# Performance work log

Hardware: AMD Instinct MI355X
Metric: run time of the kernel (lower is better)

Reference implementation:

```python
import jax, jax.numpy as jnp
import numpy as np

MEAN = jnp.array([0.4914, 0.4822, 0.4465], dtype=jnp.float32)
STD = jnp.array([0.2023, 0.1994, 0.201], dtype=jnp.float32)


def conv2d(x, w, b, stride, pad):
    out = jax.lax.conv_general_dilated(
        x, w, (stride, stride), [(pad, pad), (pad, pad)],
        dimension_numbers=('NCHW', 'OIHW', 'NCHW'))
    return out + b[None, :, None, None]


def topk_select(out_list, scores):
    # SubNet zeros the lowest int(0.75*N) |scores|; SelectNet gathers the
    # surviving channels in original channel order.
    N = scores.shape[1]
    keep = N - int(0.75 * N)
    _, idx = jax.lax.top_k(scores, keep)
    idx = jnp.sort(idx, axis=1)  # boolean-mask gather preserves order
    if out_list.ndim == 4:
        return jnp.take_along_axis(out_list, idx[:, :, None, None], axis=1)
    return jnp.take_along_axis(out_list, idx, axis=1)


def moe_conv(x, We, be, Wr, br, stride, pad):
    B = x.shape[0]
    out = conv2d(x, We.reshape((-1,) + We.shape[2:]), be.reshape(-1), stride, pad)
    scores = jnp.abs(x.reshape(B, -1) @ Wr + br)
    return topk_select(out, scores)


def moe_linear(x, We, be, Wr, br):
    out = (jnp.einsum('bi,eoi->beo', x, We) + be[None]).reshape(x.shape[0], -1)
    scores = jnp.abs(x @ Wr + br)
    return topk_select(out, scores)


def setup_inputs():
    key = jax.random.key(0)
    ks = iter(jax.random.split(key, 32))

    def w(shape, fan_in):
        return jax.random.normal(next(ks), shape, jnp.float32) / np.sqrt(fan_in)

    B = 1024
    inp = {'x': jax.random.uniform(next(ks), (B, 3, 32, 32), jnp.float32)}
    inp['W0'] = w((32, 3, 3, 3), 27);        inp['b0'] = jnp.zeros((32,), jnp.float32)
    inp['W2'] = w((32, 32, 4, 4), 512);      inp['b2'] = jnp.zeros((32,), jnp.float32)
    inp['W4'] = w((64, 32, 3, 3), 288);      inp['b4'] = jnp.zeros((64,), jnp.float32)
    inp['W6e'] = w((4, 64, 64, 4, 4), 1024); inp['b6e'] = jnp.zeros((4, 64), jnp.float32)
    inp['Wr6'] = w((64 * 16 * 16, 256), 16384); inp['br6'] = jnp.zeros((256,), jnp.float32)
    inp['W9e'] = w((4, 512, 4096), 4096);    inp['b9e'] = jnp.zeros((4, 512), jnp.float32)
    inp['Wr9'] = w((4096, 2048), 4096);      inp['br9'] = jnp.zeros((2048,), jnp.float32)
    inp['W11e'] = w((4, 512, 512), 512);     inp['b11e'] = jnp.zeros((4, 512), jnp.float32)
    inp['Wr11'] = w((512, 2048), 512);       inp['br11'] = jnp.zeros((2048,), jnp.float32)
    inp['W13e'] = w((4, 10, 512), 512);      inp['b13e'] = jnp.zeros((4, 10), jnp.float32)
    inp['Wr13'] = w((512, 40), 512);         inp['br13'] = jnp.zeros((40,), jnp.float32)
    return inp


def reference(x, W0, b0, W2, b2, W4, b4,
              W6e, b6e, Wr6, br6,
              W9e, b9e, Wr9, br9,
              W11e, b11e, Wr11, br11,
              W13e, b13e, Wr13, br13):
    x = (x - MEAN[None, :, None, None]) / STD[None, :, None, None]
    out = jax.nn.relu(conv2d(x, W0, b0, 1, 1))      # [B,32,32,32]
    out = jax.nn.relu(conv2d(out, W2, b2, 2, 1))    # [B,32,16,16]
    out = jax.nn.relu(conv2d(out, W4, b4, 1, 1))    # [B,64,16,16]
    out = jax.nn.relu(moe_conv(out, W6e, b6e, Wr6, br6, 2, 1))  # [B,64,8,8]
    out = out.reshape(out.shape[0], -1)             # [B,4096]
    out = jax.nn.relu(moe_linear(out, W9e, b9e, Wr9, br9))      # [B,512]
    out = jax.nn.relu(moe_linear(out, W11e, b11e, Wr11, br11))  # [B,512]
    return moe_linear(out, W13e, b13e, Wr13, br13)  # [B,10]
```

## Files before the change

kernel.cpp:

```cpp
#include <hip/hip_runtime.h>
#include <stdint.h>

#define DEV __device__ __forceinline__

typedef __attribute__((ext_vector_type(8))) short bf16x8;
typedef __attribute__((ext_vector_type(8))) unsigned short u16x8;
typedef __attribute__((ext_vector_type(4))) float f32x4;

DEV unsigned short rne1(float f, float& rem) {
  uint32_t u = __float_as_uint(f);
  uint32_t t = (u + 0x7fffu + ((u >> 16) & 1u)) & 0xffff0000u;
  rem = f - __uint_as_float(t);
  return (unsigned short)(t >> 16);
}
DEV void split3(float f, unsigned short& a0, unsigned short& a1, unsigned short& a2) {
  float r1, r2;
  a0 = rne1(f, r1);
  a1 = rne1(r1, r2);
  uint32_t u = __float_as_uint(r2);
  a2 = (unsigned short)((u + 0x7fffu + ((u >> 16) & 1u)) >> 16);
}
DEV void split3_4(float4 v, ushort4& h0, ushort4& h1, ushort4& h2) {
  split3(v.x, h0.x, h1.x, h2.x);
  split3(v.y, h0.y, h1.y, h2.y);
  split3(v.z, h0.z, h1.z, h2.z);
  split3(v.w, h0.w, h1.w, h2.w);
}

__global__ __launch_bounds__(256) void k_conv0(
    const float* __restrict__ x, const float* __restrict__ W,
    const float* __restrict__ b, float* __restrict__ y0, int base)
{
  __shared__ float sIn[3][34][34];
  const int t = threadIdx.x;
  const long img = base + blockIdx.x;
  const float mean[3] = {0.4914f, 0.4822f, 0.4465f};
  const float stdv[3] = {0.2023f, 0.1994f, 0.201f};
  for (int i = t; i < 3 * 34 * 34; i += 256) {
    int c = i / 1156, r = i % 1156, yy = r / 34 - 1, xx = r % 34 - 1;
    float v = 0.f;
    if ((unsigned)yy < 32u && (unsigned)xx < 32u)
      v = (x[((img * 3 + c) * 32 + yy) * 32 + xx] - mean[c]) / stdv[c];
    (&sIn[0][0][0])[i] = v;
  }
  __syncthreads();
  for (int p = t; p < 1024; p += 256) {
    const int py = p >> 5, px = p & 31;
    float in[27];
#pragma unroll
    for (int c = 0; c < 3; c++)
#pragma unroll
      for (int ky = 0; ky < 3; ky++)
#pragma unroll
        for (int kx = 0; kx < 3; kx++)
          in[c * 9 + ky * 3 + kx] = sIn[c][py + ky][px + kx];
#pragma unroll 4
    for (int oc = 0; oc < 32; oc++) {
      float acc = b[oc];
      const float* wp = W + oc * 27;
#pragma unroll
      for (int k = 0; k < 27; k++) acc += in[k] * wp[k];
      y0[(((long)blockIdx.x * 32 + oc) * 32 + py) * 32 + px] = fmaxf(acc, 0.f);
    }
  }
}

__global__ __launch_bounds__(256, 4) void k_conv2(
    const float* __restrict__ y0, const float* __restrict__ W,
    const float* __restrict__ b, float* __restrict__ y2)
{
  __shared__ float sP[2][2][8][17][17];
  const int t = threadIdx.x;
  const int px = t & 15, py = t >> 4;
  float acc[32];
#pragma unroll
  for (int o = 0; o < 32; o++) acc[o] = b[o];
  for (int icp = 0; icp < 4; icp++) {
    __syncthreads();
    for (int i = t; i < 8 * 34 * 34; i += 256) {
      int c = i / 1156, r = i % 1156, iy = r / 34 - 1, ix = r % 34 - 1;
      float v = 0.f;
      if ((unsigned)iy < 32u && (unsigned)ix < 32u)
        v = y0[(((long)blockIdx.x * 32 + icp * 8 + c) * 32 + iy) * 32 + ix];
      sP[iy & 1][ix & 1][c][(iy + 1) >> 1][(ix + 1) >> 1] = v;
    }
    __syncthreads();
#pragma unroll 1
    for (int c = 0; c < 8; c++) {
      float in[16];
#pragma unroll
      for (int ky = 0; ky < 4; ky++)
#pragma unroll
        for (int kx = 0; kx < 4; kx++)
          in[ky * 4 + kx] = sP[(ky + 1) & 1][(kx + 1) & 1][c][py + (ky >> 1)][px + (kx >> 1)];
      const float* wp = W + (icp * 8 + c) * 16;
#pragma unroll
      for (int o = 0; o < 32; o++) {
        float s = 0.f;
#pragma unroll
        for (int k = 0; k < 16; k++)
          s += in[k] * wp[o * 512 + k];
        acc[o] += s;
      }
    }
  }
#pragma unroll
  for (int o = 0; o < 32; o++)
    y2[(((long)blockIdx.x * 32 + o) * 16 + py) * 16 + px] = fmaxf(acc[o], 0.f);
}

__global__ __launch_bounds__(256) void k_splitW4(
    const float* __restrict__ W, unsigned short* __restrict__ Wsp)
{
  const int i = blockIdx.x * 256 + threadIdx.x;
  if (i >= 64 * 288) return;
  const int o = i / 288, r = i % 288, ic = r / 9, tap = r % 9;
  unsigned short a0, a1, a2;
  split3(W[i], a0, a1, a2);
  const int base = (tap * 64 + o) * 32 + ic;
  Wsp[base] = a0;
  Wsp[18432 + base] = a1;
  Wsp[36864 + base] = a2;
}

__global__ __launch_bounds__(256, 2) void k_conv4m(
    const float* __restrict__ y2, const unsigned short* __restrict__ Wsp,
    const float* __restrict__ bb, float* __restrict__ y4)
{
  __shared__ __align__(16) unsigned short sX[3][324][40];
  const int t = threadIdx.x;
  const int lane = t & 63, wid = t >> 6;
  const int fr = lane & 15, kg = lane >> 4;
  const long img = blockIdx.x;
  const float* yimg = y2 + img * (32 * 256);

  for (int i = t; i < 324 * 32; i += 256) {
    const int ic = i / 324, pos = i % 324;
    const int iy = pos / 18, ix = pos % 18;
    float v = 0.f;
    if ((unsigned)(iy - 1) < 16u && (unsigned)(ix - 1) < 16u)
      v = yimg[(ic * 16 + iy - 1) * 16 + ix - 1];
    unsigned short a0, a1, a2;
    split3(v, a0, a1, a2);
    sX[0][pos][ic] = a0;
    sX[1][pos][ic] = a1;
    sX[2][pos][ic] = a2;
  }
  __syncthreads();

  f32x4 acc[4][4];
#pragma unroll
  for (int i = 0; i < 4; i++)
#pragma unroll
    for (int j = 0; j < 4; j++) acc[i][j] = (f32x4)0.f;

  const int pyb = wid * 4;
#pragma unroll 1
  for (int tap = 0; tap < 9; tap++) {
    const int ky = tap / 3, kx = tap % 3;
    bf16x8 bfv[3][4];
#pragma unroll
    for (int s = 0; s < 3; s++)
#pragma unroll
      for (int nf = 0; nf < 4; nf++)
        bfv[s][nf] = *(const bf16x8*)&sX[s][(pyb + nf + ky) * 18 + fr + kx][kg * 8];
#pragma unroll
    for (int mf = 0; mf < 4; mf++) {
      const int wb = (tap * 64 + mf * 16 + fr) * 32 + kg * 8;
      bf16x8 a0 = *(const bf16x8*)&Wsp[wb];
      bf16x8 a1 = *(const bf16x8*)&Wsp[18432 + wb];
      bf16x8 a2 = *(const bf16x8*)&Wsp[36864 + wb];
#pragma unroll
      for (int nf = 0; nf < 4; nf++) {
        f32x4 a = acc[mf][nf];
        a = __builtin_amdgcn_mfma_f32_16x16x32_bf16(a1, bfv[1][nf], a, 0, 0, 0);
        a = __builtin_amdgcn_mfma_f32_16x16x32_bf16(a0, bfv[2][nf], a, 0, 0, 0);
        a = __builtin_amdgcn_mfma_f32_16x16x32_bf16(a2, bfv[0][nf], a, 0, 0, 0);
        a = __builtin_amdgcn_mfma_f32_16x16x32_bf16(a1, bfv[0][nf], a, 0, 0, 0);
        a = __builtin_amdgcn_mfma_f32_16x16x32_bf16(a0, bfv[1][nf], a, 0, 0, 0);
        a = __builtin_amdgcn_mfma_f32_16x16x32_bf16(a0, bfv[0][nf], a, 0, 0, 0);
        acc[mf][nf] = a;
      }
    }
  }
#pragma unroll
  for (int mf = 0; mf < 4; mf++)
#pragma unroll
    for (int nf = 0; nf < 4; nf++) {
      const int p2 = wid * 64 + nf * 16 + fr;
#pragma unroll
      for (int reg = 0; reg < 4; reg++) {
        const int oc = mf * 16 + kg * 4 + reg;
        y4[(img * 64 + oc) * 256 + p2] = fmaxf(acc[mf][nf][reg] + bb[oc], 0.f);
      }
    }
}

__global__ __launch_bounds__(256) void k_splitW(
    const float* __restrict__ W, unsigned short* __restrict__ Wsp)
{
  const int i = (blockIdx.x * 256 + threadIdx.x) * 4;
  float4 v = *(const float4*)&W[i];
  ushort4 h0, h1, h2; split3_4(v, h0, h1, h2);
  *(ushort4*)&Wsp[i]          = h0;
  *(ushort4*)&Wsp[262144 + i] = h1;
  *(ushort4*)&Wsp[524288 + i] = h2;
}

__global__ __launch_bounds__(256) void k_conv6m(
    const float* __restrict__ y4, const unsigned short* __restrict__ Wsp,
    const float* __restrict__ bb, float* __restrict__ c6)
{
  __shared__ __align__(16) unsigned short sB[3][64][56];
  const int t = threadIdx.x;
  const int lane = t & 63, wid = t >> 6;
  const int fr = lane & 15, kg = lane >> 4;
  const long img = blockIdx.x;
  const int pix = t >> 2, q = t & 3;
  const int spy = pix >> 3, spx = pix & 7;
  const int icL = q >> 1, kyB = (q & 1) * 2;
  const float* yimg = y4 + img * (64 * 256);

  f32x4 acc[4][4];
#pragma unroll
  for (int i = 0; i < 4; i++)
#pragma unroll
    for (int j = 0; j < 4; j++) acc[i][j] = (f32x4)0.f;

#pragma unroll 1
  for (int ks = 0; ks < 32; ks++) {
    const int ic = ks * 2 + icL;
    float v[8];
#pragma unroll
    for (int j = 0; j < 8; j++) {
      const int ky = kyB + (j >> 2), kx = j & 3;
      const int iy = 2 * spy + ky - 1, ix = 2 * spx + kx - 1;
      v[j] = ((unsigned)iy < 16u && (unsigned)ix < 16u)
               ? yimg[(ic * 16 + iy) * 16 + ix] : 0.f;
    }
    u16x8 h0, h1, h2;
#pragma unroll
    for (int j = 0; j < 8; j++) {
      unsigned short a0, a1, a2;
      split3(v[j], a0, a1, a2);
      h0[j] = a0; h1[j] = a1; h2[j] = a2;
    }
    __syncthreads();
    *(u16x8*)&sB[0][pix][q * 8] = h0;
    *(u16x8*)&sB[1][pix][q * 8] = h1;
    *(u16x8*)&sB[2][pix][q * 8] = h2;
    __syncthreads();

    bf16x8 bfv[3][4];
#pragma unroll
    for (int s = 0; s < 3; s++)
#pragma unroll
      for (int nf = 0; nf < 4; nf++)
        bfv[s][nf] = *(const bf16x8*)&sB[s][nf * 16 + fr][kg * 8];

    const int kbase = ks * 32 + kg * 8;
#pragma unroll
    for (int mf = 0; mf < 4; mf++) {
      const int oc = wid * 64 + mf * 16 + fr;
      bf16x8 a0 = *(const bf16x8*)&Wsp[(long)oc * 1024 + kbase];
      bf16x8 a1 = *(const bf16x8*)&Wsp[(long)(256 + oc) * 1024 + kbase];
      bf16x8 a2 = *(const bf16x8*)&Wsp[(long)(512 + oc) * 1024 + kbase];
#pragma unroll
      for (int nf = 0; nf < 4; nf++) {
        f32x4 a = acc[mf][nf];
        a = __builtin_amdgcn_mfma_f32_16x16x32_bf16(a1, bfv[1][nf], a, 0, 0, 0);
        a = __builtin_amdgcn_mfma_f32_16x16x32_bf16(a0, bfv[2][nf], a, 0, 0, 0);
        a = __builtin_amdgcn_mfma_f32_16x16x32_bf16(a2, bfv[0][nf], a, 0, 0, 0);
        a = __builtin_amdgcn_mfma_f32_16x16x32_bf16(a1, bfv[0][nf], a, 0, 0, 0);
        a = __builtin_amdgcn_mfma_f32_16x16x32_bf16(a0, bfv[1][nf], a, 0, 0, 0);
        a = __builtin_amdgcn_mfma_f32_16x16x32_bf16(a0, bfv[0][nf], a, 0, 0, 0);
        acc[mf][nf] = a;
      }
    }
  }
#pragma unroll
  for (int mf = 0; mf < 4; mf++)
#pragma unroll
    for (int nf = 0; nf < 4; nf++) {
      const int ocb = wid * 64 + mf * 16 + kg * 4;
      const int p2 = nf * 16 + fr;
#pragma unroll
      for (int reg = 0; reg < 4; reg++) {
        const int oc = ocb + reg;
        c6[(img * 256 + oc) * 64 + p2] = acc[mf][nf][reg] + bb[oc];
      }
    }
}

template<int B_NK, int DO_ABS, int SPLITK>
__global__ __launch_bounds__(256, 4) void k_sgemm(
    const float* __restrict__ A, const float* __restrict__ Bm,
    const float* __restrict__ bias, float* __restrict__ C,
    int M, int N, int K)
{
  __shared__ float As[16][68];
  __shared__ float Bs[16][68];
  const int t = threadIdx.x;
  const int tx = t & 15, ty = t >> 4;
  const int n0 = blockIdx.x * 64, m0 = blockIdx.y * 64;
  const int Kc = K / SPLITK;
  const int k0 = blockIdx.z * Kc;
  float acc[4][4] = {{0.f}};
  for (int kt = 0; kt < Kc; kt += 16) {
    __syncthreads();
    {
      const int kc = t & 15, r0 = t >> 4;
#pragma unroll
      for (int i = 0; i < 4; i++)
        As[kc][r0 + 16 * i] = A[(long)(m0 + r0 + 16 * i) * K + k0 + kt + kc];
      if (B_NK) {
#pragma unroll
        for (int i = 0; i < 4; i++)
          Bs[kc][r0 + 16 * i] = Bm[(long)(n0 + r0 + 16 * i) * K + k0 + kt + kc];
      } else {
        const int nc = t & 63, kr0 = t >> 6;
#pragma unroll
        for (int i = 0; i < 4; i++)
          Bs[kr0 + 4 * i][nc] = Bm[(long)(k0 + kt + kr0 + 4 * i) * N + n0 + nc];
      }
    }
    __syncthreads();
    float part[4][4] = {{0.f}};
#pragma unroll
    for (int k = 0; k < 16; k++) {
      float4 av = *(const float4*)&As[k][ty * 4];
      float4 bv = *(const float4*)&Bs[k][tx * 4];
      const float a[4] = {av.x, av.y, av.z, av.w};
      const float bb[4] = {bv.x, bv.y, bv.z, bv.w};
#pragma unroll
      for (int i = 0; i < 4; i++)
#pragma unroll
        for (int j = 0; j < 4; j++)
          part[i][j] += a[i] * bb[j];
    }
#pragma unroll
    for (int i = 0; i < 4; i++)
#pragma unroll
      for (int j = 0; j < 4; j++)
        acc[i][j] += part[i][j];
  }
#pragma unroll
  for (int i = 0; i < 4; i++) {
    const long m = m0 + ty * 4 + i;
    float vv[4];
#pragma unroll
    for (int j = 0; j < 4; j++) {
      float u = acc[i][j];
      if (SPLITK == 1) {
        u += bias[n0 + tx * 4 + j];
        if (DO_ABS) u = fabsf(u);
      }
      vv[j] = u;
    }
    float4 v; v.x = vv[0]; v.y = vv[1]; v.z = vv[2]; v.w = vv[3];
    float* dst = (SPLITK == 1) ? &C[m * N + n0 + tx * 4]
                               : &C[((long)blockIdx.z * M + m) * N + n0 + tx * 4];
    *(float4*)dst = v;
  }
}

template<int B_NK, int DO_ABS, int SPLITK>
__global__ __launch_bounds__(256, 2) void k_mgemm(
    const float* __restrict__ A, const float* __restrict__ Bm,
    const float* __restrict__ bias, float* __restrict__ C,
    int M, int N, int K)
{
  __shared__ __align__(16) unsigned short sA[3][64][40];
  __shared__ __align__(16) unsigned short sB[3][128][40];
  const int t = threadIdx.x;
  const int n0 = blockIdx.x * 128, m0 = blockIdx.y * 64;
  const int Kc = K / SPLITK;
  const int k0 = blockIdx.z * Kc;
  const int lane = t & 63, wid = t >> 6;
  const int wm = wid >> 1, wn = wid & 1;
  const int fr = lane & 15, kg = lane >> 4;

  f32x4 acc[2][4];
#pragma unroll
  for (int i = 0; i < 2; i++)
#pragma unroll
    for (int j = 0; j < 4; j++) acc[i][j] = (f32x4)0.f;

  for (int kt = 0; kt < Kc; kt += 32) {
    __syncthreads();
    {
      const int kq = t & 7, r = t >> 3;
#pragma unroll
      for (int i = 0; i < 2; i++) {
        float4 v = *(const float4*)&A[(long)(m0 + r + 32 * i) * K + k0 + kt + kq * 4];
        ushort4 h0, h1, h2; split3_4(v, h0, h1, h2);
        *(ushort4*)&sA[0][r + 32 * i][kq * 4] = h0;
        *(ushort4*)&sA[1][r + 32 * i][kq * 4] = h1;
        *(ushort4*)&sA[2][r + 32 * i][kq * 4] = h2;
      }
    }
    if (B_NK) {
      const int kq = t & 7, r = t >> 3;
#pragma unroll
      for (int i = 0; i < 4; i++) {
        float4 v = *(const float4*)&Bm[(long)(n0 + r + 32 * i) * K + k0 + kt + kq * 4];
        ushort4 h0, h1, h2; split3_4(v, h0, h1, h2);
        *(ushort4*)&sB[0][r + 32 * i][kq * 4] = h0;
        *(ushort4*)&sB[1][r + 32 * i][kq * 4] = h1;
        *(ushort4*)&sB[2][r + 32 * i][kq * 4] = h2;
      }
    } else {
      const int nq = t & 31, kr = t >> 5;
#pragma unroll
      for (int i = 0; i < 4; i++) {
        const int k = kr + 8 * i;
        float4 v = *(const float4*)&Bm[(long)(k0 + kt + k) * N + n0 + nq * 4];
        ushort4 h0, h1, h2; split3_4(v, h0, h1, h2);
        sB[0][nq * 4 + 0][k] = h0.x; sB[1][nq * 4 + 0][k] = h1.x; sB[2][nq * 4 + 0][k] = h2.x;
        sB[0][nq * 4 + 1][k] = h0.y; sB[1][nq * 4 + 1][k] = h1.y; sB[2][nq * 4 + 1][k] = h2.y;
        sB[0][nq * 4 + 2][k] = h0.z; sB[1][nq * 4 + 2][k] = h1.z; sB[2][nq * 4 + 2][k] = h2.z;
        sB[0][nq * 4 + 3][k] = h0.w; sB[1][nq * 4 + 3][k] = h1.w; sB[2][nq * 4 + 3][k] = h2.w;
      }
    }
    __syncthreads();

    bf16x8 af[3][2], bfv[3][4];
#pragma unroll
    for (int s = 0; s < 3; s++)
#pragma unroll
      for (int mf = 0; mf < 2; mf++)
        af[s][mf] = *(const bf16x8*)&sA[s][wm * 32 + mf * 16 + fr][kg * 8];
#pragma unroll
    for (int s = 0; s < 3; s++)
#pragma unroll
      for (int nf = 0; nf < 4; nf++)
        bfv[s][nf] = *(const bf16x8*)&sB[s][wn * 64 + nf * 16 + fr][kg * 8];

#pragma unroll
    for (int mf = 0; mf < 2; mf++)
#pragma unroll
      for (int nf = 0; nf < 4; nf++) {
        f32x4 a = acc[mf][nf];
        a = __builtin_amdgcn_mfma_f32_16x16x32_bf16(af[1][mf], bfv[1][nf], a, 0, 0, 0);
        a = __builtin_amdgcn_mfma_f32_16x16x32_bf16(af[0][mf], bfv[2][nf], a, 0, 0, 0);
        a = __builtin_amdgcn_mfma_f32_16x16x32_bf16(af[2][mf], bfv[0][nf], a, 0, 0, 0);
        a = __builtin_amdgcn_mfma_f32_16x16x32_bf16(af[1][mf], bfv[0][nf], a, 0, 0, 0);
        a = __builtin_amdgcn_mfma_f32_16x16x32_bf16(af[0][mf], bfv[1][nf], a, 0, 0, 0);
        a = __builtin_amdgcn_mfma_f32_16x16x32_bf16(af[0][mf], bfv[0][nf], a, 0, 0, 0);
        acc[mf][nf] = a;
      }
  }

  float* dst = (SPLITK == 1) ? C : C + (long)blockIdx.z * M * N;
#pragma unroll
  for (int mf = 0; mf < 2; mf++)
#pragma unroll
    for (int nf = 0; nf < 4; nf++) {
      const int n = n0 + wn * 64 + nf * 16 + fr;
      const int mb = m0 + wm * 32 + mf * 16 + kg * 4;
#pragma unroll
      for (int reg = 0; reg < 4; reg++) {
        float u = acc[mf][nf][reg];
        if (SPLITK == 1) {
          u += bias[n];
          if (DO_ABS) u = fabsf(u);
        }
        dst[(long)(mb + reg) * N + n] = u;
      }
    }
}

__global__ __launch_bounds__(256) void k_reduce6(
    const float* __restrict__ part, const float* __restrict__ br,
    float* __restrict__ s6, int rows)
{
  const int i = blockIdx.x * 256 + threadIdx.x;
  const int tot = rows * 256;
  if (i < tot) {
    float s = br[i & 255];
#pragma unroll
    for (int z = 0; z < 16; z++) s += part[z * tot + i];
    s6[i] = fabsf(s);
  }
}

__global__ __launch_bounds__(256) void k_reduce9(
    const float* __restrict__ part, const float* __restrict__ br,
    float* __restrict__ s9)
{
  const int i = blockIdx.x * 256 + threadIdx.x;
  const int tot = 1024 * 2048;
  s9[i] = fabsf(part[i] + part[tot + i] + br[i & 2047]);
}

DEV int blk_reduce(int v, volatile int* sW4) {
#pragma unroll
  for (int d = 32; d > 0; d >>= 1) v += __shfl_down(v, d);
  const int lane = threadIdx.x & 63, wid = threadIdx.x >> 6;
  if (lane == 0) sW4[wid] = v;
  __syncthreads();
  int tot = sW4[0] + sW4[1] + sW4[2] + sW4[3];
  __syncthreads();
  return tot;
}

DEV int blk_exscan(int v, volatile int* sW4) {
  const int lane = threadIdx.x & 63, wid = threadIdx.x >> 6;
  int inc = v;
#pragma unroll
  for (int d = 1; d < 64; d <<= 1) {
    int u = __shfl_up(inc, d);
    if (lane >= d) inc += u;
  }
  if (lane == 63) sW4[wid] = inc;
  __syncthreads();
  int off = 0;
#pragma unroll
  for (int w = 0; w < 3; w++)
    if (w < wid) off += sW4[w];
  __syncthreads();
  return off + inc - v;
}

template<int N, int KEEP, int SPATIAL>
__global__ __launch_bounds__(256) void k_topk(
    const float* __restrict__ scores, const float* __restrict__ full,
    float* __restrict__ out)
{
  constexpr int E = N / 256;
  __shared__ int sW4[4];
  __shared__ int sSel[KEEP];
  const int t = threadIdx.x;
  const long row = blockIdx.x;
  uint32_t kk[E];
#pragma unroll
  for (int e = 0; e < E; e++) kk[e] = __float_as_uint(scores[row * N + t * E + e]);
  uint32_t prefix = 0u;
  for (int bit = 31; bit >= 0; bit--) {
    uint32_t cand = prefix | (1u << bit);
    int c = 0;
#pragma unroll
    for (int e = 0; e < E; e++) c += (kk[e] >= cand) ? 1 : 0;
    if (blk_reduce(c, sW4) >= KEEP) prefix = cand;
  }
  int myG = 0, myE = 0;
#pragma unroll
  for (int e = 0; e < E; e++) { myG += kk[e] > prefix; myE += kk[e] == prefix; }
  const int G = blk_reduce(myG, sW4);
  const int needEq = KEEP - G;
  const int prefE = blk_exscan(myE, sW4);
  const int keepcnt = myG + max(0, min(myE, needEq - prefE));
  int pos = blk_exscan(keepcnt, sW4);
  int eqSeen = prefE;
#pragma unroll
  for (int e = 0; e < E; e++) {
    const bool kp = (kk[e] > prefix) || ((kk[e] == prefix) && (eqSeen < needEq));
    if (kk[e] == prefix) eqSeen++;
    if (kp) sSel[pos++] = t * E + e;
  }
  __syncthreads();
  if (SPATIAL) {
    for (int i = t; i < KEEP * 64; i += 256)
      out[row * (KEEP * 64) + i] = fmaxf(full[(row * N + sSel[i >> 6]) * 64 + (i & 63)], 0.f);
  } else {
    for (int i = t; i < KEEP; i += 256)
      out[row * KEEP + i] = fmaxf(full[row * N + sSel[i]], 0.f);
  }
}

__global__ __launch_bounds__(256) void k_final(
    const float* __restrict__ y11, const float* __restrict__ W13,
    const float* __restrict__ b13, const float* __restrict__ Wr13,
    const float* __restrict__ br13, float* __restrict__ outp)
{
  __shared__ float sX[512];
  __shared__ float sL[64];
  __shared__ float sS[64];
  const int t = threadIdx.x;
  const long row = blockIdx.x;
  for (int i = t; i < 512; i += 256) sX[i] = y11[row * 512 + i];
  __syncthreads();
  if (t < 40) {
    float acc = b13[t];
    const float4* w4 = (const float4*)(W13 + t * 512);
    for (int k = 0; k < 128; k++) {
      float4 w = w4[k];
      acc += sX[4 * k] * w.x + sX[4 * k + 1] * w.y + sX[4 * k + 2] * w.z + sX[4 * k + 3] * w.w;
    }
    sL[t] = acc;
  } else if (t >= 64 && t < 104) {
    const int n = t - 64;
    float acc = br13[n];
    for (int k = 0; k < 512; k++) acc += sX[k] * Wr13[k * 40 + n];
    sS[n] = fabsf(acc);
  }
  __syncthreads();
  if (t < 64) {
    const uint32_t key = (t < 40) ? __float_as_uint(sS[t]) : 0u;
    uint32_t prefix = 0u;
#pragma unroll
    for (int bit = 31; bit >= 0; bit--) {
      uint32_t cand = prefix | (1u << bit);
      unsigned long long m = __ballot(t < 40 && key >= cand);
      if (__popcll(m) >= 10) prefix = cand;
    }
    const int G = __popcll(__ballot(t < 40 && key > prefix));
    const int needEq = 10 - G;
    const unsigned long long me = __ballot(t < 40 && key == prefix);
    const unsigned long long lt = (t == 0) ? 0ull : (~0ull >> (64 - t));
    const int eqr = __popcll(me & lt);
    const bool kp = (t < 40) && ((key > prefix) || (key == prefix && eqr < needEq));
    const int pos = __popcll(__ballot(kp) & lt);
    if (kp) outp[row * 10 + pos] = sL[t];
  }
}

extern "C" void kernel_launch(void* const* d_in, const int* in_sizes, int n_in,
                              void* d_out, int out_size, void* d_ws, size_t ws_size,
                              hipStream_t stream)
{
  const float* x    = (const float*)d_in[0];
  const float* W0   = (const float*)d_in[1];
  const float* b0   = (const float*)d_in[2];
  const float* W2   = (const float*)d_in[3];
  const float* b2   = (const float*)d_in[4];
  const float* W4   = (const float*)d_in[5];
  const float* b4   = (const float*)d_in[6];
  const float* W6   = (const float*)d_in[7];
  const float* b6   = (const float*)d_in[8];
  const float* Wr6  = (const float*)d_in[9];
  const float* br6  = (const float*)d_in[10];
  const float* W9   = (const float*)d_in[11];
  const float* b9   = (const float*)d_in[12];
  const float* Wr9  = (const float*)d_in[13];
  const float* br9  = (const float*)d_in[14];
  const float* W11  = (const float*)d_in[15];
  const float* b11  = (const float*)d_in[16];
  const float* Wr11 = (const float*)d_in[17];
  const float* br11 = (const float*)d_in[18];
  const float* W13  = (const float*)d_in[19];
  const float* b13  = (const float*)d_in[20];
  const float* Wr13 = (const float*)d_in[21];
  const float* br13 = (const float*)d_in[22];
  float* out = (float*)d_out;
  float* ws = (float*)d_ws;

  float* R0  = ws;
  float* R1  = ws + 16777216;
  float* y6  = ws + 16777216 + 4194304;
  float* y0c = R0;
  float* y4c = R0;
  float* c6c = R0 + 8388608;
  unsigned short* Wsp4 = (unsigned short*)(R0 + 10485760);
  float* y2c = R1;
  float* s6  = R1;
  float* p6  = R1 + 262144;
  unsigned short* Wsp = (unsigned short*)(R1 + 2359296);
  float* l9  = R0;
  float* s9  = R0 + 2097152;
  float* y9  = R0 + 4194304;
  float* l11 = R0 + 4718592;
  float* s11 = R0 + 6815744;
  float* y11 = R0 + 8912896;
  float* p9  = R0 + 9437184;

  for (int chunk = 0; chunk < 2; chunk++) {
    const int base = chunk * 512;
    k_conv0<<<512, 256, 0, stream>>>(x, W0, b0, y0c, base);
    k_conv2<<<512, 256, 0, stream>>>(y0c, W2, b2, y2c);
    k_splitW4<<<72, 256, 0, stream>>>(W4, Wsp4);
    k_conv4m<<<512, 256, 0, stream>>>(y2c, Wsp4, b4, y4c);
    k_splitW<<<256, 256, 0, stream>>>(W6, Wsp);
    k_conv6m<<<512, 256, 0, stream>>>(y4c, Wsp, b6, c6c);
    dim3 g6(256 / 64, 512 / 64, 16);
    k_sgemm<0, 0, 16><<<g6, 256, 0, stream>>>(y4c, Wr6, nullptr, p6, 512, 256, 16384);
    k_reduce6<<<512, 256, 0, stream>>>(p6, br6, s6, 512);
    k_topk<256, 64, 1><<<512, 256, 0, stream>>>(s6, c6c, y6 + (long)base * 4096);
  }

  dim3 g9m(16, 16, 1);
  k_mgemm<1, 0, 1><<<g9m, 256, 0, stream>>>(y6, W9, b9, l9, 1024, 2048, 4096);
  dim3 gs9(2048 / 64, 1024 / 64, 2);
  k_sgemm<0, 0, 2><<<gs9, 256, 0, stream>>>(y6, Wr9, nullptr, p9, 1024, 2048, 4096);
  k_reduce9<<<8192, 256, 0, stream>>>(p9, br9, s9);
  k_topk<2048, 512, 0><<<1024, 256, 0, stream>>>(s9, l9, y9);

  k_mgemm<1, 0, 1><<<g9m, 256, 0, stream>>>(y9, W11, b11, l11, 1024, 2048, 512);
  dim3 gs11(2048 / 64, 1024 / 64, 1);
  k_sgemm<0, 1, 1><<<gs11, 256, 0, stream>>>(y9, Wr11, br11, s11, 1024, 2048, 512);
  k_topk<2048, 512, 0><<<1024, 256, 0, stream>>>(s11, l11, y11);

  k_final<<<1024, 256, 0, stream>>>(y11, W13, b13, Wr13, br13, out);
}
```

Before: 1.610 ms.

## Port conv2 to bf16x3 split MFMA implicit GEMM

Replaces the scalar FP32 stride-2 4x4 conv2 kernel with an implicit-GEMM kernel on MFMA bf16 instructions. Each input and weight value is split into three bf16 parts and six cross-product MFMAs recover near-FP32 accuracy. The aim is to move the conv arithmetic off the vector ALUs onto matrix cores. In exchange it adds per-element split work, im2col staging through shared memory and uncoalesced global reads of the input.

```diff
diff --git a/kernel.cpp b/kernel.cpp
--- a/kernel.cpp
+++ b/kernel.cpp
@@ -65,48 +65,96 @@
   }
 }
 
-__global__ __launch_bounds__(256, 4) void k_conv2(
-    const float* __restrict__ y0, const float* __restrict__ W,
-    const float* __restrict__ b, float* __restrict__ y2)
-{
-  __shared__ float sP[2][2][8][17][17];
+__global__ __launch_bounds__(256, 2) void k_conv2m(
+    const float* __restrict__ y0, const float* __restrict__ W2,
+    const float* __restrict__ bb, float* __restrict__ y2)
+{
+  __shared__ __align__(16) unsigned short sB[3][256][40];
   const int t = threadIdx.x;
-  const int px = t & 15, py = t >> 4;
-  float acc[32];
-#pragma unroll
-  for (int o = 0; o < 32; o++) acc[o] = b[o];
-  for (int icp = 0; icp < 4; icp++) {
+  const int lane = t & 63, wid = t >> 6;
+  const int fr = lane & 15, kg = lane >> 4;
+  const long img = blockIdx.x;
+  const int py = t >> 4, px = t & 15;
+  const float* yimg = y0 + img * (32 * 1024);
+
+  f32x4 acc[2][4];
+#pragma unroll
+  for (int i = 0; i < 2; i++)
+#pragma unroll
+    for (int j = 0; j < 4; j++) acc[i][j] = (f32x4)0.f;
+
+#pragma unroll 1
+  for (int ks = 0; ks < 16; ks++) {
     __syncthreads();
-    for (int i = t; i < 8 * 34 * 34; i += 256) {
-      int c = i / 1156, r = i % 1156, iy = r / 34 - 1, ix = r % 34 - 1;
-      float v = 0.f;
-      if ((unsigned)iy < 32u && (unsigned)ix < 32u)
-        v = y0[(((long)blockIdx.x * 32 + icp * 8 + c) * 32 + iy) * 32 + ix];
-      sP[iy & 1][ix & 1][c][(iy + 1) >> 1][(ix + 1) >> 1] = v;
+#pragma unroll
+    for (int icL = 0; icL < 2; icL++) {
+      const int ic = ks * 2 + icL;
+#pragma unroll
+      for (int ky = 0; ky < 4; ky++) {
+        const int iy = 2 * py + ky - 1;
+        float v[4];
+#pragma unroll
+        for (int kx = 0; kx < 4; kx++) {
+          const int ix = 2 * px + kx - 1;
+          v[kx] = ((unsigned)iy < 32u && (unsigned)ix < 32u)
+                    ? yimg[(ic * 32 + iy) * 32 + ix] : 0.f;
+        }
+        ushort4 h0, h1, h2;
+        split3_4(make_float4(v[0], v[1], v[2], v[3]), h0, h1, h2);
+        const int kloc = icL * 16 + ky * 4;
+        *(ushort4*)&sB[0][t][kloc] = h0;
+        *(ushort4*)&sB[1][t][kloc] = h1;
+        *(ushort4*)&sB[2][t][kloc] = h2;
+      }
     }
     __syncthreads();
-#pragma unroll 1
-    for (int c = 0; c < 8; c++) {
-      float in[16];
-#pragma unroll
-      for (int ky = 0; ky < 4; ky++)
-#pragma unroll
-        for (int kx = 0; kx < 4; kx++)
-          in[ky * 4 + kx] = sP[(ky + 1) & 1][(kx + 1) & 1][c][py + (ky >> 1)][px + (kx >> 1)];
-      const float* wp = W + (icp * 8 + c) * 16;
-#pragma unroll
-      for (int o = 0; o < 32; o++) {
-        float s = 0.f;
-#pragma unroll
-        for (int k = 0; k < 16; k++)
-          s += in[k] * wp[o * 512 + k];
-        acc[o] += s;
-      }
-    }
-  }
-#pragma unroll
-  for (int o = 0; o < 32; o++)
-    y2[(((long)blockIdx.x * 32 + o) * 16 + py) * 16 + px] = fmaxf(acc[o], 0.f);
+
+    bf16x8 bfv[3][4];
+#pragma unroll
+    for (int s = 0; s < 3; s++)
+#pragma unroll
+      for (int nf = 0; nf < 4; nf++)
+        bfv[s][nf] = *(const bf16x8*)&sB[s][wid * 64 + nf * 16 + fr][kg * 8];
+
+#pragma unroll
+    for (int mf = 0; mf < 2; mf++) {
+      const float* wr = W2 + (long)(mf * 16 + fr) * 512 + ks * 32 + kg * 8;
+      float4 w0 = *(const float4*)wr;
+      float4 w1 = *(const float4*)(wr + 4);
+      ushort4 p0, p1, p2, q0, q1, q2;
+      split3_4(w0, p0, p1, p2);
+      split3_4(w1, q0, q1, q2);
+      bf16x8 a0, a1, a2;
+      a0[0]=(short)p0.x; a0[1]=(short)p0.y; a0[2]=(short)p0.z; a0[3]=(short)p0.w;
+      a0[4]=(short)q0.x; a0[5]=(short)q0.y; a0[6]=(short)q0.z; a0[7]=(short)q0.w;
+      a1[0]=(short)p1.x; a1[1]=(short)p1.y; a1[2]=(short)p1.z; a1[3]=(short)p1.w;
+      a1[4]=(short)q1.x; a1[5]=(short)q1.y; a1[6]=(short)q1.z; a1[7]=(short)q1.w;
+      a2[0]=(short)p2.x; a2[1]=(short)p2.y; a2[2]=(short)p2.z; a2[3]=(short)p2.w;
+      a2[4]=(short)q2.x; a2[5]=(short)q2.y; a2[6]=(short)q2.z; a2[7]=(short)q2.w;
+#pragma unroll
+      for (int nf = 0; nf < 4; nf++) {
+        f32x4 a = acc[mf][nf];
+        a = __builtin_amdgcn_mfma_f32_16x16x32_bf16(a1, bfv[1][nf], a, 0, 0, 0);
+        a = __builtin_amdgcn_mfma_f32_16x16x32_bf16(a0, bfv[2][nf], a, 0, 0, 0);
+        a = __builtin_amdgcn_mfma_f32_16x16x32_bf16(a2, bfv[0][nf], a, 0, 0, 0);
+        a = __builtin_amdgcn_mfma_f32_16x16x32_bf16(a1, bfv[0][nf], a, 0, 0, 0);
+        a = __builtin_amdgcn_mfma_f32_16x16x32_bf16(a0, bfv[1][nf], a, 0, 0, 0);
+        a = __builtin_amdgcn_mfma_f32_16x16x32_bf16(a0, bfv[0][nf], a, 0, 0, 0);
+        acc[mf][nf] = a;
+      }
+    }
+  }
+#pragma unroll
+  for (int mf = 0; mf < 2; mf++)
+#pragma unroll
+    for (int nf = 0; nf < 4; nf++) {
+      const int pix = wid * 64 + nf * 16 + fr;
+#pragma unroll
+      for (int reg = 0; reg < 4; reg++) {
+        const int oc = mf * 16 + kg * 4 + reg;
+        y2[(img * 32 + oc) * 256 + pix] = fmaxf(acc[mf][nf][reg] + bb[oc], 0.f);
+      }
+    }
 }
 
 __global__ __launch_bounds__(256) void k_splitW4(
@@ -667,7 +715,7 @@
   for (int chunk = 0; chunk < 2; chunk++) {
     const int base = chunk * 512;
     k_conv0<<<512, 256, 0, stream>>>(x, W0, b0, y0c, base);
-    k_conv2<<<512, 256, 0, stream>>>(y0c, W2, b2, y2c);
+    k_conv2m<<<512, 256, 0, stream>>>(y0c, W2, b2, y2c);
     k_splitW4<<<72, 256, 0, stream>>>(W4, Wsp4);
     k_conv4m<<<512, 256, 0, stream>>>(y2c, Wsp4, b4, y4c);
     k_splitW<<<256, 256, 0, stream>>>(W6, Wsp);
```

New measurement: 1.397 ms. 1.15x faster.
